# Kernel tuning notes

Hardware: AMD Instinct MI355X
Metric: run time of the kernel (lower is better)

## Reference

```python
import jax, jax.numpy as jnp
import numpy as np

A_COEF, B_COEF, C_COEF = 1.0, 0.1, 10.0
KL_COEF = 0.005
EPS = 1e-6

B, P1, F, P2 = 32, 778, 1538, 3000
PARAM_DIM, LATENT = 61, 64


def setup_inputs() -> dict:
    key = jax.random.key(0)
    ks = jax.random.split(key, 9)
    return {
        "recon_x": jax.random.normal(ks[0], (B, PARAM_DIM), jnp.float32),
        "x": jax.random.normal(ks[1], (B, PARAM_DIM), jnp.float32),
        "mu": jax.random.normal(ks[2], (B, LATENT), jnp.float32),
        "logvar": jax.random.normal(ks[3], (B, LATENT), jnp.float32),
        "recon_xyz": jax.random.normal(ks[4], (B, P1, 3), jnp.float32),
        "hand_xyz": jax.random.normal(ks[5], (B, P1, 3), jnp.float32),
        "hand_faces": jax.random.randint(ks[6], (B, F, 3), 0, P1, jnp.int64),
        "obj_pts": jax.random.normal(ks[7], (B, P2, 3), jnp.float32),
        "v_weights": jax.random.uniform(ks[8], (P1,), jnp.float32),
    }


def _verts_normals_single(verts, faces):
    # verts: (V,3), faces: (F,3). PyTorch3D-style area-weighted vertex normals.
    v0 = verts[faces[:, 0]]
    v1 = verts[faces[:, 1]]
    v2 = verts[faces[:, 2]]
    fn = jnp.cross(v1 - v0, v2 - v0)  # (F,3) ~ 2*area*face_normal
    n = (jnp.zeros_like(verts)
         .at[faces[:, 0]].add(fn)
         .at[faces[:, 1]].add(fn)
         .at[faces[:, 2]].add(fn))
    norm = jnp.linalg.norm(n, axis=-1, keepdims=True)
    return n / jnp.maximum(norm, EPS)


_verts_normals = jax.vmap(_verts_normals_single)


def _sqdist(xp, yp):
    # (B,P1,P2) pairwise squared distances
    x2 = jnp.sum(xp * xp, axis=-1)[:, :, None]
    y2 = jnp.sum(yp * yp, axis=-1)[:, None, :]
    return x2 + y2 - 2.0 * jnp.einsum('bpd,bqd->bpq', xp, yp)


def _point2point_signed(xp, yp, x_normals):
    # xp: (B,P1,3) hand, yp: (B,P2,3) object, x_normals: (B,P1,3)
    d2 = _sqdist(xp, yp)
    xidx = jnp.argmin(d2, axis=2)  # (B,P1) nearest object point per hand vert
    yidx = jnp.argmin(d2, axis=1)  # (B,P2) nearest hand vert per object point
    x_near = jnp.take_along_axis(yp, xidx[..., None], axis=1)  # (B,P1,3)
    y_near = jnp.take_along_axis(xp, yidx[..., None], axis=1)  # (B,P2,3)
    x2y = xp - x_near
    y2x = yp - y_near
    y_nn = jnp.take_along_axis(x_normals, yidx[..., None], axis=1)  # (B,P2,3)
    in_out = jnp.sign(jnp.sum(y_nn * y2x, axis=-1))
    y2x_signed = jnp.linalg.norm(y2x, axis=2) * in_out  # (B,P2)
    x2y_signed = jnp.linalg.norm(x2y, axis=2)           # (B,P1)
    return y2x_signed, x2y_signed


def _loss_cnet(verts_rhand, verts_rhand_gt, faces, verts_obj, v_weights):
    v_w2 = jnp.power(v_weights, 1.0 / 2.5)
    rh_n = _verts_normals(verts_rhand, faces)
    rh_n_gt = _verts_normals(verts_rhand_gt, faces)
    o2h, h2o = _point2point_signed(verts_rhand, verts_obj, rh_n)
    o2h_gt, h2o_gt = _point2point_signed(verts_rhand_gt, verts_obj, rh_n_gt)
    w_dist = (o2h_gt < 0.01) & (o2h_gt > -0.005)
    w_neg = o2h < 0.0
    w = jnp.where(w_neg, 1.5, jnp.where(w_dist, 1.0, 0.1))
    loss_h = 35.0 * (1.0 - KL_COEF) * jnp.mean(jnp.abs(jnp.abs(h2o) - jnp.abs(h2o_gt)) * v_w2)
    loss_o = 30.0 * (1.0 - KL_COEF) * jnp.mean(jnp.abs(o2h - o2h_gt) * w)
    return loss_h + loss_o


def reference(recon_x, x, mu, logvar, recon_xyz, hand_xyz, hand_faces, obj_pts, v_weights):
    bsz = recon_x.shape[0]
    param_loss = jnp.sum((recon_x - x) ** 2) / bsz
    recon_loss = jnp.sum((recon_xyz - hand_xyz) ** 2) / hand_xyz.shape[0]
    KLD = -0.5 * jnp.sum(1.0 + logvar - mu ** 2 - jnp.exp(logvar)) / hand_xyz.shape[0]
    cvae_loss = recon_loss + KLD
    ho_loss = _loss_cnet(recon_xyz, hand_xyz, hand_faces, obj_pts, v_weights)
    loss = A_COEF * cvae_loss + B_COEF * param_loss + C_COEF * ho_loss
    return loss, param_loss, ho_loss, recon_loss, KLD
```

## Files before the change

kernel.cpp:

```cpp
#include <hip/hip_runtime.h>
#include <math.h>

#define B 32
#define P1 778
#define NF 1538
#define P2 3000
#define PARAM_DIM 61
#define LATENT 64

#define P1PAD 784
#define NTH 49
#define CHO 192
#define NTO 12
#define NCH 16
#define NPART 16

#define RED1_BLKS 16
#define HC_BLKS 128
#define OC_BLKS 192
#define HALF_F 769

#define D1_NRM 128
#define D1_TOT (D1_NRM + RED1_BLKS)
#define D2_TOT (NCH * 64)
#define D3_TOT (OC_BLKS + HC_BLKS)

#define NP_OFF  0
#define NP_SZ   (2*2*B*P1*4)
#define OS_OFF  (NP_OFF + NP_SZ)
#define OS_SZ   (2*B*P2)
#define HP_OFF  (OS_OFF + OS_SZ)
#define HP_SZ   (NPART*2*B*P1PAD)
#define R1_OFF  (HP_OFF + HP_SZ)
#define RH_OFF  (R1_OFF + RED1_BLKS*3)
#define RO_OFF  (RH_OFF + HC_BLKS)

typedef __attribute__((ext_vector_type(8))) short bf16x8;
typedef __attribute__((ext_vector_type(4))) float f32x4;
union U4 { uint4 u; bf16x8 v; };

static __device__ __forceinline__ unsigned umin2(unsigned a, unsigned b) { return a < b ? a : b; }
static __device__ __forceinline__ unsigned bhi(float x) { return __float_as_uint(x) >> 16; }
static __device__ __forceinline__ float bres(float x, unsigned h) { return x - __uint_as_float(h << 16); }

__global__ __launch_bounds__(256) void kd1(
    const float* __restrict__ recon_x, const float* __restrict__ x,
    const float* __restrict__ mu, const float* __restrict__ logvar,
    const float* __restrict__ recon_xyz, const float* __restrict__ hand_xyz,
    const int* __restrict__ faces, float* __restrict__ ws) {
  __shared__ float4 sv[P1];
  __shared__ float sn[4][2336];
  const int tid = threadIdx.x;
  const int bid = blockIdx.x;

  if (bid < D1_NRM) {
    const int half = bid >> 6, r = bid & 63, set = r >> 5, b = r & 31;
    const float* verts = (set == 0 ? recon_xyz : hand_xyz) + b * P1 * 3;
    const int* f = faces + b * NF * 3 + half * HALF_F * 3;
    const int nf = (half == 0) ? HALF_F : (NF - HALF_F);
    for (int i = tid; i < P1; i += 256)
      sv[i] = make_float4(verts[3*i], verts[3*i+1], verts[3*i+2], 0.f);
    for (int i = tid; i < 4 * 2336; i += 256) ((float*)sn)[i] = 0.f;
    __syncthreads();
    float* s = sn[tid >> 6];
    for (int k = tid; k < nf; k += 256) {
      int i0 = f[3*k], i1 = f[3*k+1], i2 = f[3*k+2];
      float4 v0 = sv[i0], v1 = sv[i1], v2 = sv[i2];
      float e0x = v1.x - v0.x, e0y = v1.y - v0.y, e0z = v1.z - v0.z;
      float e1x = v2.x - v0.x, e1y = v2.y - v0.y, e1z = v2.z - v0.z;
      float fx = e0y * e1z - e0z * e1y;
      float fy = e0z * e1x - e0x * e1z;
      float fz = e0x * e1y - e0y * e1x;
      atomicAdd(&s[3*i0+0], fx); atomicAdd(&s[3*i0+1], fy); atomicAdd(&s[3*i0+2], fz);
      atomicAdd(&s[3*i1+0], fx); atomicAdd(&s[3*i1+1], fy); atomicAdd(&s[3*i1+2], fz);
      atomicAdd(&s[3*i2+0], fx); atomicAdd(&s[3*i2+1], fy); atomicAdd(&s[3*i2+2], fz);
    }
    __syncthreads();
    float4* np = (float4*)(ws + NP_OFF) + (size_t)((half * 2 + set) * B + b) * P1;
    for (int p = tid; p < P1; p += 256) {
      float nx = sn[0][3*p] + sn[1][3*p] + sn[2][3*p] + sn[3][3*p];
      float ny = sn[0][3*p+1] + sn[1][3*p+1] + sn[2][3*p+1] + sn[3][3*p+1];
      float nz = sn[0][3*p+2] + sn[1][3*p+2] + sn[2][3*p+2] + sn[3][3*p+2];
      np[p] = make_float4(nx, ny, nz, 0.f);
    }
  } else {
    const int blk = bid - D1_NRM;
    const int gtid = blk * 256 + tid, stride = RED1_BLKS * 256;
    float sp = 0.f, sr = 0.f, sk = 0.f;
    for (int i = gtid; i < B * PARAM_DIM; i += stride) { float d = recon_x[i] - x[i]; sp += d * d; }
    for (int i = gtid; i < B * P1 * 3; i += stride)    { float d = recon_xyz[i] - hand_xyz[i]; sr += d * d; }
    for (int i = gtid; i < B * LATENT; i += stride)    { float lv = logvar[i], m = mu[i]; sk += 1.f + lv - m * m - expf(lv); }
    for (int off = 32; off > 0; off >>= 1) {
      sp += __shfl_down(sp, off, 64);
      sr += __shfl_down(sr, off, 64);
      sk += __shfl_down(sk, off, 64);
    }
    float* sred = (float*)sn;
    const int wv = tid >> 6;
    if ((tid & 63) == 0) { sred[wv*3] = sp; sred[wv*3+1] = sr; sred[wv*3+2] = sk; }
    __syncthreads();
    if (tid == 0) {
      float a = 0.f, bb = 0.f, c = 0.f;
      for (int w = 0; w < 4; ++w) { a += sred[w*3]; bb += sred[w*3+1]; c += sred[w*3+2]; }
      ws[R1_OFF + blk*3+0] = a; ws[R1_OFF + blk*3+1] = bb; ws[R1_OFF + blk*3+2] = c;
    }
  }
}

__global__ __launch_bounds__(256, 4) void kd2(
    const float* __restrict__ recon_xyz, const float* __restrict__ hand_xyz,
    const float* __restrict__ obj, float* __restrict__ ws) {
  __shared__ float4 sObj[CHO];
  __shared__ uint4  sPack4[(NTH + 4) * 32];
  __shared__ unsigned sKeys[4][CHO];
  __shared__ uint4  sZero;

  const int tid = threadIdx.x;
  const int bid = blockIdx.x;
  const int chunk = bid >> 6, rr = bid & 63, set = rr >> 5, b = rr & 31;
  const float* verts = (set == 0 ? recon_xyz : hand_xyz) + b * P1 * 3;
  const float* op = obj + (size_t)b * P2 * 3;

  if (tid == 0) sZero = make_uint4(0u, 0u, 0u, 0u);
  for (int i = tid; i < CHO; i += 256) {
    const int q = chunk * CHO + i;
    float ox, oy, oz;
    if (q < P2) { ox = op[3*q]; oy = op[3*q+1]; oz = op[3*q+2]; }
    else        { ox = oy = oz = 1.0e6f; }
    sObj[i] = make_float4(ox, oy, oz, ox*ox + oy*oy + oz*oz);
  }
  for (int idx = tid; idx < NTH * 32; idx += 256) {
    const int t = idx >> 5, vl = idx & 31, vg = vl >> 4;
    const int i = t * 16 + (vl & 15);
    float vx, vy, vz;
    if (i < P1) { vx = verts[3*i]; vy = verts[3*i+1]; vz = verts[3*i+2]; }
    else        { vx = vy = vz = 1.0e6f; }
    const float sx = -2.f * vx, sy = -2.f * vy, sz = -2.f * vz;
    const unsigned hx = bhi(sx), hy = bhi(sy), hz = bhi(sz);
    unsigned w0, w1, w2, w3;
    if (vg == 0) {
      const unsigned lx = bhi(bres(sx, hx));
      const unsigned ly = bhi(bres(sy, hy));
      const unsigned lz = bhi(bres(sz, hz));
      w0 = hx | (hy << 16);
      w1 = hz | (lx << 16);
      w2 = ly | (lz << 16);
      w3 = hx | (hy << 16);
    } else {
      const float h2 = vx*vx + vy*vy + vz*vz;
      const unsigned h2h = bhi(h2);
      const unsigned h2l = bhi(bres(h2, h2h));
      w0 = hz  | (h2h << 16);
      w1 = h2l | (0x3F80u << 16);
      w2 = 0x3F80u;
      w3 = 0u;
    }
    sPack4[t * 32 + vl] = make_uint4(w0, w1, w2, w3);
  }
  __syncthreads();

  const int l = tid & 63, wv = tid >> 6, g = l >> 4, cl = l & 15;
  U4 bw[NTO];
  #pragma unroll
  for (int j = 0; j < NTO; ++j) {
    const float4 o = sObj[j * 16 + cl];
    unsigned u0 = 0u, u1 = 0u, u2 = 0u, u3 = 0u;
    if (g == 0) {
      const unsigned ohx = bhi(o.x), ohy = bhi(o.y), ohz = bhi(o.z);
      const unsigned olx = bhi(bres(o.x, ohx));
      const unsigned oly = bhi(bres(o.y, ohy));
      u0 = ohx | (ohy << 16);
      u1 = ohz | (ohx << 16);
      u2 = ohy | (ohz << 16);
      u3 = olx | (oly << 16);
    } else if (g == 1) {
      const unsigned ohz = bhi(o.z);
      const unsigned olz = bhi(bres(o.z, ohz));
      const float o2p = o.w + 1.0f;
      const unsigned o2h = bhi(o2p);
      const unsigned o2l = bhi(bres(o2p, o2h));
      u0 = olz | (0x3F80u << 16);
      u1 = 0x3F80u | (o2h << 16);
      u2 = o2l;
      u3 = 0u;
    }
    bw[j].u = make_uint4(u0, u1, u2, u3);
  }

  unsigned om[NTO];
  #pragma unroll
  for (int j = 0; j < NTO; ++j) om[j] = 0xFFFFFFFFu;

  float* hpart = ws + HP_OFF + (size_t)(((chunk * 2) + set) * B + b) * P1PAD;
  const f32x4 czero = {0.f, 0.f, 0.f, 0.f};
  const int nt = (NTH - wv + 3) >> 2;

  const uint4* ap = (l < 32) ? ((const uint4*)sPack4 + wv * 32 + l) : &sZero;
  const int astep = (l < 32) ? 4 * 32 : 0;
  uint4 au = *ap; ap += astep;

  for (int s = 0; s < nt; ++s) {
    const int ib = (wv + 4 * s) * 16 + g * 4;
    const uint4 aunx = *ap; ap += astep;
    U4 ac; ac.u = au;
    float hm0 = 3.0e38f, hm1 = 3.0e38f, hm2 = 3.0e38f, hm3 = 3.0e38f;
    #pragma unroll
    for (int j = 0; j < NTO; ++j) {
      const f32x4 d = __builtin_amdgcn_mfma_f32_16x16x32_bf16(ac.v, bw[j].v, czero, 0, 0, 0);
      hm0 = fminf(hm0, d[0]); hm1 = fminf(hm1, d[1]);
      hm2 = fminf(hm2, d[2]); hm3 = fminf(hm3, d[3]);
      const unsigned k0 = (__float_as_uint(d[0]) & 0xFFFFFC00u) | (unsigned)(ib + 0);
      const unsigned k1 = (__float_as_uint(d[1]) & 0xFFFFFC00u) | (unsigned)(ib + 1);
      const unsigned k2 = (__float_as_uint(d[2]) & 0xFFFFFC00u) | (unsigned)(ib + 2);
      const unsigned k3 = (__float_as_uint(d[3]) & 0xFFFFFC00u) | (unsigned)(ib + 3);
      om[j] = umin2(om[j], umin2(umin2(k0, k1), umin2(k2, k3)));
    }
    #pragma unroll
    for (int m = 1; m <= 8; m <<= 1) {
      hm0 = fminf(hm0, __shfl_xor(hm0, m, 64));
      hm1 = fminf(hm1, __shfl_xor(hm1, m, 64));
      hm2 = fminf(hm2, __shfl_xor(hm2, m, 64));
      hm3 = fminf(hm3, __shfl_xor(hm3, m, 64));
    }
    if (cl == 0)
      *(float4*)&hpart[ib] = make_float4(hm0 - 1.f, hm1 - 1.f, hm2 - 1.f, hm3 - 1.f);
    au = aunx;
  }

  #pragma unroll
  for (int j = 0; j < NTO; ++j) {
    unsigned v = umin2(om[j], (unsigned)__shfl_xor((int)om[j], 16, 64));
    v = umin2(v, (unsigned)__shfl_xor((int)v, 32, 64));
    if (l < 16) sKeys[wv][j * 16 + l] = v;
  }
  __syncthreads();

  const float4* np0 = (const float4*)(ws + NP_OFF) + (size_t)(set * B + b) * P1;
  const float4* np1 = np0 + (size_t)2 * B * P1;
  float* os = ws + OS_OFF + (size_t)(set * B + b) * P2;
  for (int i = tid; i < CHO; i += 256) {
    const int q = chunk * CHO + i;
    if (q < P2) {
      const unsigned key = umin2(umin2(sKeys[0][i], sKeys[1][i]),
                                 umin2(sKeys[2][i], sKeys[3][i]));
      int hi = (int)(key & 1023u); if (hi > P1 - 1) hi = P1 - 1;
      const float hx = verts[3*hi], hy = verts[3*hi+1], hz = verts[3*hi+2];
      const float4 o = sObj[i];
      const float dx = o.x - hx, dy = o.y - hy, dz = o.z - hz;
      const float d2 = fmaf(dx, dx, fmaf(dy, dy, dz * dz));
      const float4 na = np0[hi], nb = np1[hi];
      const float nx = na.x + nb.x, ny = na.y + nb.y, nz = na.z + nb.z;
      const float dt = nx * dx + ny * dy + nz * dz;
      const float sg = (dt > 0.f) ? 1.f : ((dt < 0.f) ? -1.f : 0.f);
      os[q] = sqrtf(d2) * sg;
    }
  }
}

__global__ __launch_bounds__(256) void kd3(const float* __restrict__ vw,
                                           float* __restrict__ ws) {
  __shared__ float sred[4];
  const int tid = threadIdx.x;
  const int bid = blockIdx.x;
  if (bid < OC_BLKS) {
    const int gtid = bid * 256 + tid, stride = OC_BLKS * 256;
    float so = 0.f;
    for (int i = gtid; i < B * P2; i += stride) {
      float osA = ws[OS_OFF + i];
      float osB = ws[OS_OFF + (size_t)B * P2 + i];
      bool wdist = (osB < 0.01f) && (osB > -0.005f);
      float w = (osA < 0.f) ? 1.5f : (wdist ? 1.f : 0.1f);
      so += fabsf(osA - osB) * w;
    }
    for (int off = 32; off > 0; off >>= 1) so += __shfl_down(so, off, 64);
    if ((tid & 63) == 0) sred[tid >> 6] = so;
    __syncthreads();
    if (tid == 0) ws[RO_OFF + bid] = sred[0] + sred[1] + sred[2] + sred[3];
  } else {
    const int blk = bid - OC_BLKS;
    const int gtid = blk * 256 + tid, stride = HC_BLKS * 256;
    float sh = 0.f;
    for (int i = gtid; i < B * P1; i += stride) {
      const int p = i % P1, bb = i / P1;
      const size_t base0 = (size_t)HP_OFF + (size_t)bb * P1PAD + p;
      float m0 = 3.0e38f, m1 = 3.0e38f;
      #pragma unroll
      for (int c = 0; c < NPART; ++c) {
        m0 = fminf(m0, ws[base0 + (size_t)(c*2+0) * B * P1PAD]);
        m1 = fminf(m1, ws[base0 + (size_t)(c*2+1) * B * P1PAD]);
      }
      m0 = fmaxf(m0, 0.f); m1 = fmaxf(m1, 0.f);
      sh += fabsf(sqrtf(m0) - sqrtf(m1)) * powf(vw[p], 0.4f);
    }
    for (int off = 32; off > 0; off >>= 1) sh += __shfl_down(sh, off, 64);
    if ((tid & 63) == 0) sred[tid >> 6] = sh;
    __syncthreads();
    if (tid == 0) ws[RH_OFF + blk] = sred[0] + sred[1] + sred[2] + sred[3];
  }
}

__global__ void kfin(const float* __restrict__ ws, float* __restrict__ out) {
  const int lane = threadIdx.x;
  float sp = 0.f, sr = 0.f, sk = 0.f, sh = 0.f, so = 0.f;
  for (int i = lane; i < RED1_BLKS; i += 64) {
    sp += ws[R1_OFF + i*3+0]; sr += ws[R1_OFF + i*3+1]; sk += ws[R1_OFF + i*3+2];
  }
  for (int i = lane; i < HC_BLKS; i += 64) sh += ws[RH_OFF + i];
  for (int i = lane; i < OC_BLKS; i += 64) so += ws[RO_OFF + i];
  for (int off = 32; off > 0; off >>= 1) {
    sp += __shfl_down(sp, off, 64);
    sr += __shfl_down(sr, off, 64);
    sk += __shfl_down(sk, off, 64);
    sh += __shfl_down(sh, off, 64);
    so += __shfl_down(so, off, 64);
  }
  if (lane == 0) {
    float param_loss = sp / (float)B;
    float recon_loss = sr / (float)B;
    float KLD = -0.5f * sk / (float)B;
    float cvae = recon_loss + KLD;
    float loss_h = 35.f * (1.f - 0.005f) * sh / (float)(B * P1);
    float loss_o = 30.f * (1.f - 0.005f) * so / (float)(B * P2);
    float ho = loss_h + loss_o;
    out[0] = cvae + 0.1f * param_loss + 10.f * ho;
    out[1] = param_loss;
    out[2] = ho;
    out[3] = recon_loss;
    out[4] = KLD;
  }
}

extern "C" void kernel_launch(void* const* d_in, const int* in_sizes, int n_in,
                              void* d_out, int out_size, void* d_ws, size_t ws_size,
                              hipStream_t stream) {
  const float* recon_x   = (const float*)d_in[0];
  const float* x         = (const float*)d_in[1];
  const float* mu        = (const float*)d_in[2];
  const float* logvar    = (const float*)d_in[3];
  const float* recon_xyz = (const float*)d_in[4];
  const float* hand_xyz  = (const float*)d_in[5];
  const int*   faces     = (const int*)d_in[6];
  const float* obj       = (const float*)d_in[7];
  const float* vw        = (const float*)d_in[8];
  float* ws = (float*)d_ws;
  float* out = (float*)d_out;

  kd1<<<dim3(D1_TOT), 256, 0, stream>>>(recon_x, x, mu, logvar,
                                        recon_xyz, hand_xyz, faces, ws);
  kd2<<<dim3(D2_TOT), 256, 0, stream>>>(recon_xyz, hand_xyz, obj, ws);
  kd3<<<dim3(D3_TOT), 256, 0, stream>>>(vw, ws);
  kfin<<<1, 64, 0, stream>>>(ws, out);
}
```

Before: 124.1 us.

## Shrink object chunk, raise occupancy, and build bf16 A-fragments on the fly

Cuts the object chunk per block from 192 to 128 points, which drops the register-held B fragments from 12 to 8, raises the chunk count to 24 and the launch-bounds occupancy hint to 6. The precomputed packed bf16 A-operand array in LDS is replaced by a plain float4 vertex array, and the hi/lo bf16 split is recomputed inside the MMA loop for each tile. The final nearest-vertex gather now reads from LDS instead of global memory. This trades more ALU work per tile and more blocks with more partial minima to reduce for less register pressure and better latency hiding.

```diff
diff --git a/kernel.cpp b/kernel.cpp
--- a/kernel.cpp
+++ b/kernel.cpp
@@ -10,10 +10,10 @@
 
 #define P1PAD 784
 #define NTH 49
-#define CHO 192
-#define NTO 12
-#define NCH 16
-#define NPART 16
+#define CHO 128
+#define NTO 8
+#define NCH 24
+#define NPART NCH
 
 #define RED1_BLKS 16
 #define HC_BLKS 128
@@ -107,13 +107,12 @@
   }
 }
 
-__global__ __launch_bounds__(256, 4) void kd2(
+__global__ __launch_bounds__(256, 6) void kd2(
     const float* __restrict__ recon_xyz, const float* __restrict__ hand_xyz,
     const float* __restrict__ obj, float* __restrict__ ws) {
+  __shared__ float4 sVerts[P1PAD];
   __shared__ float4 sObj[CHO];
-  __shared__ uint4  sPack4[(NTH + 4) * 32];
   __shared__ unsigned sKeys[4][CHO];
-  __shared__ uint4  sZero;
 
   const int tid = threadIdx.x;
   const int bid = blockIdx.x;
@@ -121,41 +120,18 @@
   const float* verts = (set == 0 ? recon_xyz : hand_xyz) + b * P1 * 3;
   const float* op = obj + (size_t)b * P2 * 3;
 
-  if (tid == 0) sZero = make_uint4(0u, 0u, 0u, 0u);
+  for (int i = tid; i < P1PAD; i += 256) {
+    float vx, vy, vz;
+    if (i < P1) { vx = verts[3*i]; vy = verts[3*i+1]; vz = verts[3*i+2]; }
+    else        { vx = vy = vz = 1.0e6f; }
+    sVerts[i] = make_float4(vx, vy, vz, vx*vx + vy*vy + vz*vz);
+  }
   for (int i = tid; i < CHO; i += 256) {
     const int q = chunk * CHO + i;
     float ox, oy, oz;
     if (q < P2) { ox = op[3*q]; oy = op[3*q+1]; oz = op[3*q+2]; }
     else        { ox = oy = oz = 1.0e6f; }
     sObj[i] = make_float4(ox, oy, oz, ox*ox + oy*oy + oz*oz);
-  }
-  for (int idx = tid; idx < NTH * 32; idx += 256) {
-    const int t = idx >> 5, vl = idx & 31, vg = vl >> 4;
-    const int i = t * 16 + (vl & 15);
-    float vx, vy, vz;
-    if (i < P1) { vx = verts[3*i]; vy = verts[3*i+1]; vz = verts[3*i+2]; }
-    else        { vx = vy = vz = 1.0e6f; }
-    const float sx = -2.f * vx, sy = -2.f * vy, sz = -2.f * vz;
-    const unsigned hx = bhi(sx), hy = bhi(sy), hz = bhi(sz);
-    unsigned w0, w1, w2, w3;
-    if (vg == 0) {
-      const unsigned lx = bhi(bres(sx, hx));
-      const unsigned ly = bhi(bres(sy, hy));
-      const unsigned lz = bhi(bres(sz, hz));
-      w0 = hx | (hy << 16);
-      w1 = hz | (lx << 16);
-      w2 = ly | (lz << 16);
-      w3 = hx | (hy << 16);
-    } else {
-      const float h2 = vx*vx + vy*vy + vz*vz;
-      const unsigned h2h = bhi(h2);
-      const unsigned h2l = bhi(bres(h2, h2h));
-      w0 = hz  | (h2h << 16);
-      w1 = h2l | (0x3F80u << 16);
-      w2 = 0x3F80u;
-      w3 = 0u;
-    }
-    sPack4[t * 32 + vl] = make_uint4(w0, w1, w2, w3);
   }
   __syncthreads();
 
@@ -195,14 +171,30 @@
   const f32x4 czero = {0.f, 0.f, 0.f, 0.f};
   const int nt = (NTH - wv + 3) >> 2;
 
-  const uint4* ap = (l < 32) ? ((const uint4*)sPack4 + wv * 32 + l) : &sZero;
-  const int astep = (l < 32) ? 4 * 32 : 0;
-  uint4 au = *ap; ap += astep;
-
   for (int s = 0; s < nt; ++s) {
-    const int ib = (wv + 4 * s) * 16 + g * 4;
-    const uint4 aunx = *ap; ap += astep;
-    U4 ac; ac.u = au;
+    const int t = wv + 4 * s;
+    const int ib = t * 16 + g * 4;
+    U4 ac;
+    if (l < 32) {
+      const float4 v = sVerts[t * 16 + cl];
+      if (g == 0) {
+        const float sx = -2.f * v.x, sy = -2.f * v.y, sz = -2.f * v.z;
+        const unsigned hx = bhi(sx), hy = bhi(sy), hz = bhi(sz);
+        const unsigned lx = bhi(bres(sx, hx));
+        const unsigned ly = bhi(bres(sy, hy));
+        const unsigned lz = bhi(bres(sz, hz));
+        ac.u = make_uint4(hx | (hy << 16), hz | (lx << 16),
+                          ly | (lz << 16), hx | (hy << 16));
+      } else {
+        const float sz = -2.f * v.z;
+        const unsigned hz = bhi(sz);
+        const unsigned h2h = bhi(v.w);
+        const unsigned h2l = bhi(bres(v.w, h2h));
+        ac.u = make_uint4(hz | (h2h << 16), h2l | (0x3F80u << 16), 0x3F80u, 0u);
+      }
+    } else {
+      ac.u = make_uint4(0u, 0u, 0u, 0u);
+    }
     float hm0 = 3.0e38f, hm1 = 3.0e38f, hm2 = 3.0e38f, hm3 = 3.0e38f;
     #pragma unroll
     for (int j = 0; j < NTO; ++j) {
@@ -224,7 +216,6 @@
     }
     if (cl == 0)
       *(float4*)&hpart[ib] = make_float4(hm0 - 1.f, hm1 - 1.f, hm2 - 1.f, hm3 - 1.f);
-    au = aunx;
   }
 
   #pragma unroll
@@ -244,9 +235,9 @@
       const unsigned key = umin2(umin2(sKeys[0][i], sKeys[1][i]),
                                  umin2(sKeys[2][i], sKeys[3][i]));
       int hi = (int)(key & 1023u); if (hi > P1 - 1) hi = P1 - 1;
-      const float hx = verts[3*hi], hy = verts[3*hi+1], hz = verts[3*hi+2];
+      const float4 h = sVerts[hi];
       const float4 o = sObj[i];
-      const float dx = o.x - hx, dy = o.y - hy, dz = o.z - hz;
+      const float dx = o.x - h.x, dy = o.y - h.y, dz = o.z - h.z;
       const float d2 = fmaf(dx, dx, fmaf(dy, dy, dz * dz));
       const float4 na = np0[hi], nb = np1[hi];
       const float nx = na.x + nb.x, ny = na.y + nb.y, nz = na.z + nb.z;
```

After: 138.3 us. 11.5% more time.
